# Kernel tuning notes

Hardware: AMD Instinct MI355X
Metric: run time of the kernel (lower is better)

The kernel has to match this reference:

```python
import jax, jax.numpy as jnp
import numpy as np

EPS = 1e-8
TAU = 0.2
IOU_THR = 0.5
NEG = -1e9
N, C, H, D_FG, D_CLS = 8192, 1024, 256, 64, 128


def setup_inputs() -> dict:
    key = jax.random.key(0)
    ks = jax.random.split(key, 11)
    def lin(k, fan_in, fan_out):
        return jax.random.normal(k, (fan_in, fan_out), jnp.float32) / np.sqrt(fan_in)
    return {
        "roi_feats": jax.random.normal(ks[0], (N, C), jnp.float32),
        "labels": jax.random.randint(ks[1], (N,), 0, 21, jnp.int32).astype(jnp.int64),
        "ious": jax.random.uniform(ks[2], (N,), jnp.float32),
        "fg_w1": lin(ks[3], C, H), "fg_b1": jnp.zeros((H,), jnp.float32),
        "fg_w2": lin(ks[4], H, D_FG), "fg_b2": jnp.zeros((D_FG,), jnp.float32),
        "cls_w1": lin(ks[5], C, H), "cls_b1": jnp.zeros((H,), jnp.float32),
        "cls_w2": lin(ks[6], H, D_CLS), "cls_b2": jnp.zeros((D_CLS,), jnp.float32),
    }


def _project_normalize(x, w1, b1, w2, b2):
    h = jax.nn.relu(x @ w1 + b1)
    z = h @ w2 + b2
    norm = jnp.maximum(jnp.linalg.norm(z, axis=1, keepdims=True), EPS)
    return z / norm


def _forward(roi_feats, labels, ious, fg_w1, fg_b1, fg_w2, fg_b2, cls_w1, cls_b1, cls_w2, cls_b2):
    n = roi_feats.shape[0]
    z_fg = _project_normalize(roi_feats, fg_w1, fg_b1, fg_w2, fg_b2)
    z_cls = _project_normalize(roi_feats, cls_w1, cls_b1, cls_w2, cls_b2)

    ignore = labels == -1
    fg = (labels > 0) & ~ignore
    iou_weight = jnp.where(ious > IOU_THR, ious, 0.0)
    eye = jnp.eye(n, dtype=bool)

    # ---- fg/bg contrastive (bg_as_negatives_only=True) ----
    sim_fg = (z_fg @ z_fg.T) / TAU                       # [N,N]
    exp_sim = jnp.exp(sim_fg)
    denom = jnp.sum(exp_sim * (~eye).astype(jnp.float32), axis=1)
    pos = (fg & ~ignore)[None, :] & ~eye                 # positives: fg columns, no self
    n_pos = jnp.sum(pos, axis=1)
    numer = jnp.sum(exp_sim * pos.astype(jnp.float32), axis=1)
    # original computes den = denom + EPS then -log((numer+EPS)/(den+EPS))
    loss_i = -jnp.log((numer + EPS) / (denom + 2.0 * EPS))
    valid = (fg & ~ignore) & (n_pos > 0)
    w = iou_weight * valid.astype(jnp.float32)
    loss_fg_bg = jnp.sum(w * loss_i) / (jnp.sum(w) + EPS)

    # ---- class supervised contrastive ----
    sim_cls = (z_cls @ z_cls.T) / TAU
    sim_masked = jnp.where(eye, NEG, sim_cls)
    log_denom = jax.nn.logsumexp(sim_masked, axis=1)     # [N]
    log_p = jnp.where(eye, NEG, sim_cls - log_denom[:, None])
    # pos_mask keeps diagonal (as in original): same label, col not ignore, col label != 0
    posc = (labels[None, :] == labels[:, None]) & (~ignore)[None, :] & (labels[None, :] != 0)
    n_posc = jnp.sum(posc, axis=1).astype(jnp.float32)
    sum_log_p = jnp.sum(log_p * posc.astype(jnp.float32), axis=1)
    valid_c = (fg & ~ignore) & (n_posc > 0) & jnp.isfinite(log_denom)
    Lzi = jnp.where(valid_c, -sum_log_p / (n_posc + EPS), 0.0)
    wc = iou_weight * valid_c.astype(jnp.float32)
    loss_supcon = jnp.sum(wc * Lzi) / (jnp.sum(wc) + EPS)

    return jnp.stack([loss_fg_bg, loss_supcon])


def reference(roi_feats, labels, ious, fg_w1, fg_b1, fg_w2, fg_b2, cls_w1, cls_b1, cls_w2, cls_b2):
    return _forward(roi_feats, labels, ious, fg_w1, fg_b1, fg_w2, fg_b2, cls_w1, cls_b1, cls_w2, cls_b2)
```

## Files before the change

### kernel.cpp

```cpp
#include <hip/hip_runtime.h>


typedef __attribute__((ext_vector_type(8))) short bs8;
typedef __attribute__((ext_vector_type(4))) float f4;

#define MFMA_BF16(a, b, c) __builtin_amdgcn_mfma_f32_16x16x32_bf16((a), (b), (c), 0, 0, 0)

#if defined(__has_builtin)
#if __has_builtin(__builtin_amdgcn_exp2f)
#define EXP2F(x) __builtin_amdgcn_exp2f(x)
#endif
#endif
#ifndef EXP2F
#define EXP2F(x) exp2f(x)
#endif

#define K_LOG2E 7.2134752044448170f

__device__ __forceinline__ unsigned short f2bf(float f) {
  unsigned int u = __float_as_uint(f);
  u = (u + 0x7fffu + ((u >> 16) & 1u)) >> 16;
  return (unsigned short)u;
}
__device__ __forceinline__ float bf2f(unsigned short s) {
  return __uint_as_float(((unsigned int)s) << 16);
}

constexpr size_t O_W1T  = 0;
constexpr size_t O_W2TF = 1048576;
constexpr size_t O_W2TC = 1081344;
constexpr size_t O_H    = 1146880;
constexpr size_t O_ZF   = 9535488;
constexpr size_t O_ZC   = 10584064;
constexpr size_t O_SCLS = 12681216;
constexpr size_t O_ROWD = 12697600;
constexpr size_t O_ROWN = 12730368;
constexpr size_t O_ROWS = 12763136;
constexpr size_t O_SCAL = 12795904;
constexpr size_t O_HIST = 12795920;
constexpr size_t O_NFG  = 12796048;
constexpr int ZERO_WORDS = (int)((O_SCAL + 16 - O_SCLS) / 4);

__global__ void __launch_bounds__(256) prep_kernel(
    const float* __restrict__ fgw1, const float* __restrict__ clsw1,
    const float* __restrict__ fgw2, const float* __restrict__ clsw2,
    const int* __restrict__ labels,
    unsigned short* __restrict__ W1T, unsigned short* __restrict__ W2Tf,
    unsigned short* __restrict__ W2Tc,
    int* __restrict__ hist, int* __restrict__ nfg, float* __restrict__ zp) {
  const int b = blockIdx.x;
  const int t = threadIdx.x;

  if (b >= 141) {
    const int i = (b - 141) * 256 + t;
    if (i < ZERO_WORDS) zp[i] = 0.f;
    return;
  }
  if (b == 140) {
    __shared__ int sh[33];
    if (t < 33) sh[t] = 0;
    __syncthreads();
    for (int it = 0; it < 32; it++) {
      const int lab = labels[it * 256 + t];
      if (lab >= 0 && lab < 32) atomicAdd(&sh[lab], 1);
      if (lab > 0) atomicAdd(&sh[32], 1);
    }
    __syncthreads();
    if (t < 32) hist[t] = sh[t];
    if (t == 32) *nfg = sh[32];
    return;
  }
  int m, tb;
  if (b < 64)       { m = 0; tb = b; }
  else if (b < 128) { m = 1; tb = b - 64; }
  else if (b < 132) { m = 2; tb = b - 128; }
  else              { m = 3; tb = b - 132; }
  __shared__ float tile[64][65];
  const float* src;
  unsigned short* dst;
  int R, C;
  if (m == 0)      { src = fgw1;  dst = W1T;              R = 1024; C = 256; }
  else if (m == 1) { src = clsw1; dst = W1T + 256 * 1024; R = 1024; C = 256; }
  else if (m == 2) { src = fgw2;  dst = W2Tf;             R = 256;  C = 64;  }
  else             { src = clsw2; dst = W2Tc;             R = 256;  C = 128; }
  const int cT = C >> 6;
  const int r0 = (tb / cT) << 6, c0 = (tb % cT) << 6;
  {
    const int rr = t >> 4, cc = (t & 15) << 2;
#pragma unroll
    for (int i = 0; i < 4; i++) {
      float4 v = *(const float4*)(src + (size_t)(r0 + rr + i * 16) * C + c0 + cc);
      tile[rr + i * 16][cc] = v.x; tile[rr + i * 16][cc + 1] = v.y;
      tile[rr + i * 16][cc + 2] = v.z; tile[rr + i * 16][cc + 3] = v.w;
    }
  }
  __syncthreads();
  {
    const int dr = t >> 2, dc = (t & 3) << 4;
    bs8 o0, o1;
#pragma unroll
    for (int j = 0; j < 8; j++) o0[j] = (short)f2bf(tile[dc + j][dr]);
#pragma unroll
    for (int j = 0; j < 8; j++) o1[j] = (short)f2bf(tile[dc + 8 + j][dr]);
    unsigned short* dp = dst + (size_t)(c0 + dr) * R + r0 + dc;
    *(bs8*)dp = o0;
    *(bs8*)(dp + 8) = o1;
  }
}

__global__ void __launch_bounds__(256) gemm1_kernel(
    const float* __restrict__ X, const unsigned short* __restrict__ W1T,
    const float* __restrict__ b1f, const float* __restrict__ b1c,
    unsigned short* __restrict__ H) {
  __shared__ __align__(16) unsigned short lA[64 * 72];
  __shared__ __align__(16) unsigned short lB[128 * 72];
  const int t = threadIdx.x;
  const int w = t >> 6, lane = t & 63, ln = lane & 15, quad = lane >> 4;
  const int m0 = blockIdx.x * 64, n0 = blockIdx.y * 128;

  const int ar = t >> 2, ac = (t & 3) * 16;
  const int br = t >> 1, bc = (t & 1) * 32;
  const float* xbase = X + (size_t)(m0 + ar) * 1024 + ac;
  const unsigned short* bbase = W1T + (size_t)(n0 + br) * 1024 + bc;

  float4 xa[4];
  bs8 xb[4];
#pragma unroll
  for (int i = 0; i < 4; i++) xa[i] = *(const float4*)(xbase + i * 4);
#pragma unroll
  for (int i = 0; i < 4; i++) xb[i] = *(const bs8*)(bbase + i * 8);

  f4 acc[8];
#pragma unroll
  for (int s = 0; s < 8; s++) acc[s] = (f4){0.f, 0.f, 0.f, 0.f};

  for (int ks = 0; ks < 16; ks++) {
    {
      unsigned short* ap = &lA[ar * 72 + ac];
#pragma unroll
      for (int i = 0; i < 2; i++) {
        bs8 av;
        av[0] = (short)f2bf(xa[2 * i].x);     av[1] = (short)f2bf(xa[2 * i].y);
        av[2] = (short)f2bf(xa[2 * i].z);     av[3] = (short)f2bf(xa[2 * i].w);
        av[4] = (short)f2bf(xa[2 * i + 1].x); av[5] = (short)f2bf(xa[2 * i + 1].y);
        av[6] = (short)f2bf(xa[2 * i + 1].z); av[7] = (short)f2bf(xa[2 * i + 1].w);
        *(bs8*)(ap + i * 8) = av;
      }
      unsigned short* bp = &lB[br * 72 + bc];
#pragma unroll
      for (int i = 0; i < 4; i++) *(bs8*)(bp + i * 8) = xb[i];
    }
    __syncthreads();
    if (ks < 15) {
      const int k1 = (ks + 1) * 64;
#pragma unroll
      for (int i = 0; i < 4; i++) xa[i] = *(const float4*)(xbase + k1 + i * 4);
#pragma unroll
      for (int i = 0; i < 4; i++) xb[i] = *(const bs8*)(bbase + k1 + i * 8);
    }
#pragma unroll
    for (int kk = 0; kk < 2; kk++) {
      bs8 af = *(const bs8*)&lA[(w * 16 + ln) * 72 + kk * 32 + quad * 8];
#pragma unroll
      for (int s = 0; s < 8; s++) {
        bs8 bf = *(const bs8*)&lB[(s * 16 + ln) * 72 + kk * 32 + quad * 8];
        acc[s] = MFMA_BF16(af, bf, acc[s]);
      }
    }
    __syncthreads();
  }
#pragma unroll
  for (int s = 0; s < 8; s++) {
    const int n = n0 + s * 16 + ln;
    const float b = (n < 256) ? b1f[n] : b1c[n - 256];
#pragma unroll
    for (int r = 0; r < 4; r++) {
      float v = fmaxf(acc[s][r] + b, 0.f);
      H[(size_t)(m0 + w * 16 + quad * 4 + r) * 512 + n] = f2bf(v);
    }
  }
}

__global__ void __launch_bounds__(256) gemm2_kernel(
    const unsigned short* __restrict__ H,
    const unsigned short* __restrict__ W2Tf, const unsigned short* __restrict__ W2Tc,
    const float* __restrict__ b2f, const float* __restrict__ b2c,
    unsigned short* __restrict__ Zf, unsigned short* __restrict__ Zc) {
  const int t = threadIdx.x;
  const int w = t >> 6, lane = t & 63, ln = lane & 15, quad = lane >> 4;
  const int rw = blockIdx.x * 32 + (w & 1) * 16;

  if (w < 2) {
    const unsigned short* hrow = H + (size_t)(rw + ln) * 512;
    f4 acc[4];
#pragma unroll
    for (int s = 0; s < 4; s++) acc[s] = (f4){0.f, 0.f, 0.f, 0.f};
#pragma unroll
    for (int ks = 0; ks < 8; ks++) {
      bs8 af = *(const bs8*)(hrow + ks * 32 + quad * 8);
#pragma unroll
      for (int s = 0; s < 4; s++) {
        bs8 bf = *(const bs8*)(W2Tf + (size_t)(s * 16 + ln) * 256 + ks * 32 + quad * 8);
        acc[s] = MFMA_BF16(af, bf, acc[s]);
      }
    }
    float ss[4] = {0.f, 0.f, 0.f, 0.f};
#pragma unroll
    for (int s = 0; s < 4; s++) {
      float b = b2f[s * 16 + ln];
#pragma unroll
      for (int r = 0; r < 4; r++) {
        acc[s][r] += b;
        ss[r] = fmaf(acc[s][r], acc[s][r], ss[r]);
      }
    }
#pragma unroll
    for (int r = 0; r < 4; r++) {
#pragma unroll
      for (int off = 1; off < 16; off <<= 1) ss[r] += __shfl_xor(ss[r], off, 64);
      float sc = 1.f / fmaxf(sqrtf(ss[r]), 1e-8f);
#pragma unroll
      for (int s = 0; s < 4; s++)
        Zf[(size_t)(rw + quad * 4 + r) * 64 + s * 16 + ln] = f2bf(acc[s][r] * sc);
    }
  } else {
    const unsigned short* hrow = H + (size_t)(rw + ln) * 512 + 256;
    f4 acc[8];
#pragma unroll
    for (int s = 0; s < 8; s++) acc[s] = (f4){0.f, 0.f, 0.f, 0.f};
#pragma unroll
    for (int ks = 0; ks < 8; ks++) {
      bs8 af = *(const bs8*)(hrow + ks * 32 + quad * 8);
#pragma unroll
      for (int s = 0; s < 8; s++) {
        bs8 bf = *(const bs8*)(W2Tc + (size_t)(s * 16 + ln) * 256 + ks * 32 + quad * 8);
        acc[s] = MFMA_BF16(af, bf, acc[s]);
      }
    }
    float ss[4] = {0.f, 0.f, 0.f, 0.f};
#pragma unroll
    for (int s = 0; s < 8; s++) {
      float b = b2c[s * 16 + ln];
#pragma unroll
      for (int r = 0; r < 4; r++) {
        acc[s][r] += b;
        ss[r] = fmaf(acc[s][r], acc[s][r], ss[r]);
      }
    }
#pragma unroll
    for (int r = 0; r < 4; r++) {
#pragma unroll
      for (int off = 1; off < 16; off <<= 1) ss[r] += __shfl_xor(ss[r], off, 64);
      float sc = 1.f / fmaxf(sqrtf(ss[r]), 1e-8f);
#pragma unroll
      for (int s = 0; s < 8; s++)
        Zc[(size_t)(rw + quad * 4 + r) * 128 + s * 16 + ln] = f2bf(acc[s][r] * sc);
    }
  }
}

__global__ void __launch_bounds__(128) scls_kernel(const unsigned short* __restrict__ Zc,
                                                   const int* __restrict__ labels,
                                                   float* __restrict__ Scls) {
  const int c = blockIdx.x + 1;
  const int t = threadIdx.x;
  const int r0 = blockIdx.y * 256;
  float acc = 0.f;
#pragma unroll 4
  for (int r = r0; r < r0 + 256; r++) {
    if (labels[r] == c) acc += bf2f(Zc[(size_t)r * 128 + t]);
  }
  atomicAdd(&Scls[c * 128 + t], acc);
}

__global__ void __launch_bounds__(256) simfg_kernel(
    const unsigned short* __restrict__ Zf, const int* __restrict__ labels,
    float* __restrict__ rowD, float* __restrict__ rowN) {
  const int bi = blockIdx.x, d = blockIdx.y;
  if (d == 32 && bi >= 32) return;
  const int bj = (bi + d) & 63;
  const bool diag = (d == 0);

  __shared__ __align__(16) unsigned short sZf[64 * 72];
  __shared__ float sFg[64];
  __shared__ float sCol[4][2][4][16][2];
  const int t = threadIdx.x;
  const int w = t >> 6, lane = t & 63, ln = lane & 15, quad = lane >> 4;
  const int rbase = bi * 128 + w * 32;

  bs8 afg[2][2];
  float fgr[2][4];
#pragma unroll
  for (int rs = 0; rs < 2; rs++) {
    const unsigned short* zf = Zf + (size_t)(rbase + rs * 16 + ln) * 64;
#pragma unroll
    for (int s = 0; s < 2; s++) afg[rs][s] = *(const bs8*)(zf + s * 32 + quad * 8);
#pragma unroll
    for (int r = 0; r < 4; r++)
      fgr[rs][r] = (labels[rbase + rs * 16 + quad * 4 + r] > 0) ? 1.f : 0.f;
  }

  float dacc[2][4] = {}, nacc[2][4] = {};
  float cd[2][4] = {}, cn[2][4] = {};

#pragma unroll
  for (int ct = 0; ct < 2; ct++) {
    const int c0 = bj * 128 + ct * 64;
    __syncthreads();
#pragma unroll
    for (int i = 0; i < 2; i++) {
      int ch = t + i * 256;
      int j = ch >> 3, c8 = (ch & 7) * 8;
      *(bs8*)&sZf[j * 72 + c8] = *(const bs8*)(Zf + (size_t)(c0 + j) * 64 + c8);
    }
    if (t < 64) sFg[t] = (labels[c0 + t] > 0) ? 1.f : 0.f;
    __syncthreads();

#pragma unroll
    for (int s = 0; s < 4; s++) {
      const int lcol = s * 16 + ln;
      const float fgc = sFg[lcol];
      bs8 b0 = *(const bs8*)&sZf[lcol * 72 + quad * 8];
      bs8 b1 = *(const bs8*)&sZf[lcol * 72 + 32 + quad * 8];
#pragma unroll
      for (int rs = 0; rs < 2; rs++) {
        f4 c = {0.f, 0.f, 0.f, 0.f};
        c = MFMA_BF16(afg[rs][0], b0, c);
        c = MFMA_BF16(afg[rs][1], b1, c);
#pragma unroll
        for (int r = 0; r < 4; r++) {
          float e = EXP2F(c[r] * K_LOG2E);
          dacc[rs][r] += e;
          nacc[rs][r] = fmaf(fgc, e, nacc[rs][r]);
          cd[ct][s] += e;
          cn[ct][s] = fmaf(fgr[rs][r], e, cn[ct][s]);
        }
      }
    }
  }

  if (!diag) {
#pragma unroll
    for (int ct = 0; ct < 2; ct++)
#pragma unroll
      for (int s = 0; s < 4; s++) {
        float dv = cd[ct][s], nv = cn[ct][s];
#pragma unroll
        for (int off = 16; off < 64; off <<= 1) {
          dv += __shfl_xor(dv, off, 64);
          nv += __shfl_xor(nv, off, 64);
        }
        if (quad == 0) {
          sCol[w][ct][s][ln][0] = dv;
          sCol[w][ct][s][ln][1] = nv;
        }
      }
    __syncthreads();
    if (t < 128) {
      const int ct = t >> 6, s = (t >> 4) & 3, lm = t & 15;
      float dv = 0.f, nv = 0.f;
#pragma unroll
      for (int ww = 0; ww < 4; ww++) {
        dv += sCol[ww][ct][s][lm][0];
        nv += sCol[ww][ct][s][lm][1];
      }
      const int col = bj * 128 + t;
      atomicAdd(&rowD[col], dv);
      atomicAdd(&rowN[col], nv);
    }
  }

#pragma unroll
  for (int rs = 0; rs < 2; rs++)
#pragma unroll
    for (int r = 0; r < 4; r++) {
      float dv = dacc[rs][r], nv = nacc[rs][r];
#pragma unroll
      for (int off = 1; off < 16; off <<= 1) {
        dv += __shfl_xor(dv, off, 64);
        nv += __shfl_xor(nv, off, 64);
      }
      if (ln == 0) {
        int row = rbase + rs * 16 + quad * 4 + r;
        atomicAdd(&rowD[row], dv);
        atomicAdd(&rowN[row], nv);
      }
    }
}

__global__ void __launch_bounds__(256) simcls_kernel(
    const unsigned short* __restrict__ Zc, float* __restrict__ rowS) {
  const int bi = blockIdx.x, d = blockIdx.y;
  if (d == 32 && bi >= 32) return;
  const int bj = (bi + d) & 63;
  const bool diag = (d == 0);

  __shared__ __align__(16) unsigned short sZc[64 * 136];
  __shared__ float sCol[4][2][4][16];
  const int t = threadIdx.x;
  const int w = t >> 6, lane = t & 63, ln = lane & 15, quad = lane >> 4;
  const int rbase = bi * 128 + w * 32;

  bs8 acl[2][4];
#pragma unroll
  for (int rs = 0; rs < 2; rs++) {
    const unsigned short* zc = Zc + (size_t)(rbase + rs * 16 + ln) * 128;
#pragma unroll
    for (int s = 0; s < 4; s++) acl[rs][s] = *(const bs8*)(zc + s * 32 + quad * 8);
  }

  float sacc[2][4] = {};
  float cs[2][4] = {};

#pragma unroll
  for (int ct = 0; ct < 2; ct++) {
    const int c0 = bj * 128 + ct * 64;
    __syncthreads();
#pragma unroll
    for (int i = 0; i < 4; i++) {
      int ch = t + i * 256;
      int j = ch >> 4, c8 = (ch & 15) * 8;
      *(bs8*)&sZc[j * 136 + c8] = *(const bs8*)(Zc + (size_t)(c0 + j) * 128 + c8);
    }
    __syncthreads();

#pragma unroll
    for (int s = 0; s < 4; s++) {
      const int lcol = s * 16 + ln;
      bs8 bc0 = *(const bs8*)&sZc[lcol * 136 + quad * 8];
      bs8 bc1 = *(const bs8*)&sZc[lcol * 136 + 32 + quad * 8];
      bs8 bc2 = *(const bs8*)&sZc[lcol * 136 + 64 + quad * 8];
      bs8 bc3 = *(const bs8*)&sZc[lcol * 136 + 96 + quad * 8];
#pragma unroll
      for (int rs = 0; rs < 2; rs++) {
        f4 c = {0.f, 0.f, 0.f, 0.f};
        c = MFMA_BF16(acl[rs][0], bc0, c);
        c = MFMA_BF16(acl[rs][1], bc1, c);
        c = MFMA_BF16(acl[rs][2], bc2, c);
        c = MFMA_BF16(acl[rs][3], bc3, c);
#pragma unroll
        for (int r = 0; r < 4; r++) {
          float e = EXP2F(c[r] * K_LOG2E);
          sacc[rs][r] += e;
          cs[ct][s] += e;
        }
      }
    }
  }

  if (!diag) {
#pragma unroll
    for (int ct = 0; ct < 2; ct++)
#pragma unroll
      for (int s = 0; s < 4; s++) {
        float sv = cs[ct][s];
#pragma unroll
        for (int off = 16; off < 64; off <<= 1) sv += __shfl_xor(sv, off, 64);
        if (quad == 0) sCol[w][ct][s][ln] = sv;
      }
    __syncthreads();
    if (t < 128) {
      const int ct = t >> 6, s = (t >> 4) & 3, lm = t & 15;
      float sv = 0.f;
#pragma unroll
      for (int ww = 0; ww < 4; ww++) sv += sCol[ww][ct][s][lm];
      atomicAdd(&rowS[bj * 128 + t], sv);
    }
  }

#pragma unroll
  for (int rs = 0; rs < 2; rs++)
#pragma unroll
    for (int r = 0; r < 4; r++) {
      float sv = sacc[rs][r];
#pragma unroll
      for (int off = 1; off < 16; off <<= 1) sv += __shfl_xor(sv, off, 64);
      if (ln == 0)
        atomicAdd(&rowS[rbase + rs * 16 + quad * 4 + r], sv);
    }
}

__global__ void __launch_bounds__(256) finalize_kernel(
    const unsigned short* __restrict__ Zf, const unsigned short* __restrict__ Zc,
    const int* __restrict__ labels, const float* __restrict__ ious,
    const float* __restrict__ rowD, const float* __restrict__ rowN,
    const float* __restrict__ rowS, const float* __restrict__ Scls,
    const int* __restrict__ hist, const int* __restrict__ nfg,
    float* __restrict__ scal) {
  __shared__ float red[4][4];
  const int t = threadIdx.x, w = t >> 6, lane = t & 63;
  float aw0 = 0.f, al0 = 0.f, aw1 = 0.f, al1 = 0.f;
  const int NFG = *nfg;
  for (int it = 0; it < 16; it++) {
    const int i = it * 512 + blockIdx.x * 4 + w;
    const int lab = labels[i];
    if (lab > 0 && lab < 32) {
      const float iou = ious[i];
      const float iw = (iou > 0.5f) ? iou : 0.f;
      float dot = 0.f, ssq = 0.f;
#pragma unroll
      for (int p = 0; p < 2; p++) {
        const int k = lane + p * 64;
        const float z = bf2f(Zc[(size_t)i * 128 + k]);
        dot = fmaf(z, Scls[lab * 128 + k], dot);
        ssq = fmaf(z, z, ssq);
      }
      float zf = bf2f(Zf[(size_t)i * 64 + lane]);
      float ssqf = zf * zf;
#pragma unroll
      for (int off = 1; off < 64; off <<= 1) {
        dot += __shfl_xor(dot, off, 64);
        ssq += __shfl_xor(ssq, off, 64);
        ssqf += __shfl_xor(ssqf, off, 64);
      }
      if (lane == 0) {
        const float ef = EXP2F(K_LOG2E * ssqf);
        if (NFG - 1 > 0) {
          const float D = rowD[i] - ef;
          const float Nn = rowN[i] - ef;
          const float loss = logf(D + 2e-8f) - logf(Nn + 1e-8f);
          aw0 += iw;
          al0 += iw * loss;
        }
        const int npc = hist[lab];
        if (npc > 0) {
          const float S = rowS[i] - EXP2F(K_LOG2E * ssq);
          const float logden = logf(S);
          const float slp = (dot - ssq) * 5.0f - (float)(npc - 1) * logden - 1e9f;
          aw1 += iw;
          al1 += iw * (-slp / ((float)npc + 1e-8f));
        }
      }
    }
  }
  if (lane == 0) { red[w][0] = aw0; red[w][1] = al0; red[w][2] = aw1; red[w][3] = al1; }
  __syncthreads();
  if (t < 4) atomicAdd(&scal[t], red[0][t] + red[1][t] + red[2][t] + red[3][t]);
}

__global__ void writeout_kernel(const float* __restrict__ scal, float* __restrict__ out) {
  if (threadIdx.x == 0) {
    out[0] = scal[1] / (scal[0] + 1e-8f);
    out[1] = scal[3] / (scal[2] + 1e-8f);
  }
}

extern "C" void kernel_launch(void* const* d_in, const int* in_sizes, int n_in,
                              void* d_out, int out_size, void* d_ws, size_t ws_size,
                              hipStream_t stream) {
  (void)in_sizes; (void)n_in; (void)out_size; (void)ws_size;
  const float* roi    = (const float*)d_in[0];
  const int*   labels = (const int*)d_in[1];
  const float* ious   = (const float*)d_in[2];
  const float* fgw1   = (const float*)d_in[3];
  const float* fgb1   = (const float*)d_in[4];
  const float* fgw2   = (const float*)d_in[5];
  const float* fgb2   = (const float*)d_in[6];
  const float* clsw1  = (const float*)d_in[7];
  const float* clsb1  = (const float*)d_in[8];
  const float* clsw2  = (const float*)d_in[9];
  const float* clsb2  = (const float*)d_in[10];

  char* ws = (char*)d_ws;
  unsigned short* W1T  = (unsigned short*)(ws + O_W1T);
  unsigned short* W2Tf = (unsigned short*)(ws + O_W2TF);
  unsigned short* W2Tc = (unsigned short*)(ws + O_W2TC);
  unsigned short* Hb   = (unsigned short*)(ws + O_H);
  unsigned short* Zf   = (unsigned short*)(ws + O_ZF);
  unsigned short* Zc   = (unsigned short*)(ws + O_ZC);
  float* Scls = (float*)(ws + O_SCLS);
  float* rowD = (float*)(ws + O_ROWD);
  float* rowN = (float*)(ws + O_ROWN);
  float* rowS = (float*)(ws + O_ROWS);
  float* scal = (float*)(ws + O_SCAL);
  int* hist = (int*)(ws + O_HIST);
  int* nfg  = (int*)(ws + O_NFG);
  float* out = (float*)d_out;

  hipLaunchKernelGGL(prep_kernel, dim3(254), dim3(256), 0, stream,
                     fgw1, clsw1, fgw2, clsw2, labels, W1T, W2Tf, W2Tc,
                     hist, nfg, (float*)(ws + O_SCLS));
  hipLaunchKernelGGL(gemm1_kernel, dim3(128, 4), dim3(256), 0, stream,
                     roi, W1T, fgb1, clsb1, Hb);
  hipLaunchKernelGGL(gemm2_kernel, dim3(256), dim3(256), 0, stream,
                     Hb, W2Tf, W2Tc, fgb2, clsb2, Zf, Zc);
  hipLaunchKernelGGL(scls_kernel, dim3(20, 32), dim3(128), 0, stream, Zc, labels, Scls);
  hipLaunchKernelGGL(simfg_kernel, dim3(64, 33), dim3(256), 0, stream,
                     Zf, labels, rowD, rowN);
  hipLaunchKernelGGL(simcls_kernel, dim3(64, 33), dim3(256), 0, stream, Zc, rowS);
  hipLaunchKernelGGL(finalize_kernel, dim3(128), dim3(256), 0, stream,
                     Zf, Zc, labels, ious, rowD, rowN, rowS, Scls, hist, nfg, scal);
  hipLaunchKernelGGL(writeout_kernel, dim3(1), dim3(64), 0, stream, scal, out);
}
```

Baseline: 212.4 us.

## Merge fg and cls similarity kernels into one launch and widen gemm1 blocks

The two N×N similarity kernels (fg and class) become one kernel with a doubled grid. Blocks branch on blockIdx.y and reuse a shared-memory arena sized for the larger path. This removes one launch and lets both workloads run on the GPU together, at the cost of a larger LDS footprint for the fg blocks. Separately, gemm1 now uses 512 threads per block with 8 waves split as 4 row groups by 2 column halves, halving per-thread accumulators and loads to raise the number of waves in flight.

```diff
diff --git a/kernel.cpp b/kernel.cpp
--- a/kernel.cpp
+++ b/kernel.cpp
@@ -108,7 +108,7 @@
   }
 }
 
-__global__ void __launch_bounds__(256) gemm1_kernel(
+__global__ void __launch_bounds__(512) gemm1_kernel(
     const float* __restrict__ X, const unsigned short* __restrict__ W1T,
     const float* __restrict__ b1f, const float* __restrict__ b1c,
     unsigned short* __restrict__ H) {
@@ -116,67 +116,64 @@
   __shared__ __align__(16) unsigned short lB[128 * 72];
   const int t = threadIdx.x;
   const int w = t >> 6, lane = t & 63, ln = lane & 15, quad = lane >> 4;
+  const int wr = (w & 3) * 16, wc = (w >> 2) * 64;
   const int m0 = blockIdx.x * 64, n0 = blockIdx.y * 128;
 
-  const int ar = t >> 2, ac = (t & 3) * 16;
-  const int br = t >> 1, bc = (t & 1) * 32;
+  const int ar = t >> 3, ac = (t & 7) * 8;
+  const int br = t >> 2, bc = (t & 3) * 16;
   const float* xbase = X + (size_t)(m0 + ar) * 1024 + ac;
   const unsigned short* bbase = W1T + (size_t)(n0 + br) * 1024 + bc;
 
-  float4 xa[4];
-  bs8 xb[4];
-#pragma unroll
-  for (int i = 0; i < 4; i++) xa[i] = *(const float4*)(xbase + i * 4);
-#pragma unroll
-  for (int i = 0; i < 4; i++) xb[i] = *(const bs8*)(bbase + i * 8);
-
-  f4 acc[8];
-#pragma unroll
-  for (int s = 0; s < 8; s++) acc[s] = (f4){0.f, 0.f, 0.f, 0.f};
+  float4 xa[2];
+  bs8 xb[2];
+#pragma unroll
+  for (int i = 0; i < 2; i++) xa[i] = *(const float4*)(xbase + i * 4);
+#pragma unroll
+  for (int i = 0; i < 2; i++) xb[i] = *(const bs8*)(bbase + i * 8);
+
+  f4 acc[4];
+#pragma unroll
+  for (int s = 0; s < 4; s++) acc[s] = (f4){0.f, 0.f, 0.f, 0.f};
 
   for (int ks = 0; ks < 16; ks++) {
     {
-      unsigned short* ap = &lA[ar * 72 + ac];
-#pragma unroll
-      for (int i = 0; i < 2; i++) {
-        bs8 av;
-        av[0] = (short)f2bf(xa[2 * i].x);     av[1] = (short)f2bf(xa[2 * i].y);
-        av[2] = (short)f2bf(xa[2 * i].z);     av[3] = (short)f2bf(xa[2 * i].w);
-        av[4] = (short)f2bf(xa[2 * i + 1].x); av[5] = (short)f2bf(xa[2 * i + 1].y);
-        av[6] = (short)f2bf(xa[2 * i + 1].z); av[7] = (short)f2bf(xa[2 * i + 1].w);
-        *(bs8*)(ap + i * 8) = av;
-      }
+      bs8 av;
+      av[0] = (short)f2bf(xa[0].x); av[1] = (short)f2bf(xa[0].y);
+      av[2] = (short)f2bf(xa[0].z); av[3] = (short)f2bf(xa[0].w);
+      av[4] = (short)f2bf(xa[1].x); av[5] = (short)f2bf(xa[1].y);
+      av[6] = (short)f2bf(xa[1].z); av[7] = (short)f2bf(xa[1].w);
+      *(bs8*)&lA[ar * 72 + ac] = av;
       unsigned short* bp = &lB[br * 72 + bc];
-#pragma unroll
-      for (int i = 0; i < 4; i++) *(bs8*)(bp + i * 8) = xb[i];
+      *(bs8*)(bp) = xb[0];
+      *(bs8*)(bp + 8) = xb[1];
     }
     __syncthreads();
     if (ks < 15) {
       const int k1 = (ks + 1) * 64;
 #pragma unroll
-      for (int i = 0; i < 4; i++) xa[i] = *(const float4*)(xbase + k1 + i * 4);
-#pragma unroll
-      for (int i = 0; i < 4; i++) xb[i] = *(const bs8*)(bbase + k1 + i * 8);
+      for (int i = 0; i < 2; i++) xa[i] = *(const float4*)(xbase + k1 + i * 4);
+#pragma unroll
+      for (int i = 0; i < 2; i++) xb[i] = *(const bs8*)(bbase + k1 + i * 8);
     }
 #pragma unroll
     for (int kk = 0; kk < 2; kk++) {
-      bs8 af = *(const bs8*)&lA[(w * 16 + ln) * 72 + kk * 32 + quad * 8];
-#pragma unroll
-      for (int s = 0; s < 8; s++) {
-        bs8 bf = *(const bs8*)&lB[(s * 16 + ln) * 72 + kk * 32 + quad * 8];
+      bs8 af = *(const bs8*)&lA[(wr + ln) * 72 + kk * 32 + quad * 8];
+#pragma unroll
+      for (int s = 0; s < 4; s++) {
+        bs8 bf = *(const bs8*)&lB[(wc + s * 16 + ln) * 72 + kk * 32 + quad * 8];
         acc[s] = MFMA_BF16(af, bf, acc[s]);
       }
     }
     __syncthreads();
   }
 #pragma unroll
-  for (int s = 0; s < 8; s++) {
-    const int n = n0 + s * 16 + ln;
+  for (int s = 0; s < 4; s++) {
+    const int n = n0 + wc + s * 16 + ln;
     const float b = (n < 256) ? b1f[n] : b1c[n - 256];
 #pragma unroll
     for (int r = 0; r < 4; r++) {
       float v = fmaxf(acc[s][r] + b, 0.f);
-      H[(size_t)(m0 + w * 16 + quad * 4 + r) * 512 + n] = f2bf(v);
+      H[(size_t)(m0 + wr + quad * 4 + r) * 512 + n] = f2bf(v);
     }
   }
 }
@@ -273,211 +270,209 @@
   atomicAdd(&Scls[c * 128 + t], acc);
 }
 
-__global__ void __launch_bounds__(256) simfg_kernel(
-    const unsigned short* __restrict__ Zf, const int* __restrict__ labels,
-    float* __restrict__ rowD, float* __restrict__ rowN) {
-  const int bi = blockIdx.x, d = blockIdx.y;
+__global__ void __launch_bounds__(256) sim2_kernel(
+    const unsigned short* __restrict__ Zf, const unsigned short* __restrict__ Zc,
+    const int* __restrict__ labels,
+    float* __restrict__ rowD, float* __restrict__ rowN, float* __restrict__ rowS) {
+  const int bi = blockIdx.x, y = blockIdx.y;
+  const bool isfg = (y <= 32);
+  const int d = isfg ? y : y - 33;
   if (d == 32 && bi >= 32) return;
   const int bj = (bi + d) & 63;
   const bool diag = (d == 0);
 
-  __shared__ __align__(16) unsigned short sZf[64 * 72];
-  __shared__ float sFg[64];
-  __shared__ float sCol[4][2][4][16][2];
+  __shared__ __align__(16) char arena[19712];
   const int t = threadIdx.x;
   const int w = t >> 6, lane = t & 63, ln = lane & 15, quad = lane >> 4;
   const int rbase = bi * 128 + w * 32;
 
-  bs8 afg[2][2];
-  float fgr[2][4];
-#pragma unroll
-  for (int rs = 0; rs < 2; rs++) {
-    const unsigned short* zf = Zf + (size_t)(rbase + rs * 16 + ln) * 64;
-#pragma unroll
-    for (int s = 0; s < 2; s++) afg[rs][s] = *(const bs8*)(zf + s * 32 + quad * 8);
-#pragma unroll
-    for (int r = 0; r < 4; r++)
-      fgr[rs][r] = (labels[rbase + rs * 16 + quad * 4 + r] > 0) ? 1.f : 0.f;
-  }
-
-  float dacc[2][4] = {}, nacc[2][4] = {};
-  float cd[2][4] = {}, cn[2][4] = {};
-
-#pragma unroll
-  for (int ct = 0; ct < 2; ct++) {
-    const int c0 = bj * 128 + ct * 64;
-    __syncthreads();
-#pragma unroll
-    for (int i = 0; i < 2; i++) {
-      int ch = t + i * 256;
-      int j = ch >> 3, c8 = (ch & 7) * 8;
-      *(bs8*)&sZf[j * 72 + c8] = *(const bs8*)(Zf + (size_t)(c0 + j) * 64 + c8);
-    }
-    if (t < 64) sFg[t] = (labels[c0 + t] > 0) ? 1.f : 0.f;
-    __syncthreads();
-
-#pragma unroll
-    for (int s = 0; s < 4; s++) {
-      const int lcol = s * 16 + ln;
-      const float fgc = sFg[lcol];
-      bs8 b0 = *(const bs8*)&sZf[lcol * 72 + quad * 8];
-      bs8 b1 = *(const bs8*)&sZf[lcol * 72 + 32 + quad * 8];
-#pragma unroll
-      for (int rs = 0; rs < 2; rs++) {
-        f4 c = {0.f, 0.f, 0.f, 0.f};
-        c = MFMA_BF16(afg[rs][0], b0, c);
-        c = MFMA_BF16(afg[rs][1], b1, c);
-#pragma unroll
-        for (int r = 0; r < 4; r++) {
-          float e = EXP2F(c[r] * K_LOG2E);
-          dacc[rs][r] += e;
-          nacc[rs][r] = fmaf(fgc, e, nacc[rs][r]);
-          cd[ct][s] += e;
-          cn[ct][s] = fmaf(fgr[rs][r], e, cn[ct][s]);
-        }
-      }
-    }
-  }
-
-  if (!diag) {
-#pragma unroll
-    for (int ct = 0; ct < 2; ct++)
+  if (isfg) {
+    unsigned short* sZf = (unsigned short*)arena;
+    float* sFg = (float*)(arena + 9216);
+    float* sCol = (float*)(arena + 9472);
+
+    bs8 afg[2][2];
+    float fgr[2][4];
+#pragma unroll
+    for (int rs = 0; rs < 2; rs++) {
+      const unsigned short* zf = Zf + (size_t)(rbase + rs * 16 + ln) * 64;
+#pragma unroll
+      for (int s = 0; s < 2; s++) afg[rs][s] = *(const bs8*)(zf + s * 32 + quad * 8);
+#pragma unroll
+      for (int r = 0; r < 4; r++)
+        fgr[rs][r] = (labels[rbase + rs * 16 + quad * 4 + r] > 0) ? 1.f : 0.f;
+    }
+
+    float dacc[2][4] = {}, nacc[2][4] = {};
+    float cd[2][4] = {}, cn[2][4] = {};
+
+#pragma unroll
+    for (int ct = 0; ct < 2; ct++) {
+      const int c0 = bj * 128 + ct * 64;
+      __syncthreads();
+#pragma unroll
+      for (int i = 0; i < 2; i++) {
+        int ch = t + i * 256;
+        int j = ch >> 3, c8 = (ch & 7) * 8;
+        *(bs8*)&sZf[j * 72 + c8] = *(const bs8*)(Zf + (size_t)(c0 + j) * 64 + c8);
+      }
+      if (t < 64) sFg[t] = (labels[c0 + t] > 0) ? 1.f : 0.f;
+      __syncthreads();
+
 #pragma unroll
       for (int s = 0; s < 4; s++) {
-        float dv = cd[ct][s], nv = cn[ct][s];
-#pragma unroll
-        for (int off = 16; off < 64; off <<= 1) {
+        const int lcol = s * 16 + ln;
+        const float fgc = sFg[lcol];
+        bs8 b0 = *(const bs8*)&sZf[lcol * 72 + quad * 8];
+        bs8 b1 = *(const bs8*)&sZf[lcol * 72 + 32 + quad * 8];
+#pragma unroll
+        for (int rs = 0; rs < 2; rs++) {
+          f4 c = {0.f, 0.f, 0.f, 0.f};
+          c = MFMA_BF16(afg[rs][0], b0, c);
+          c = MFMA_BF16(afg[rs][1], b1, c);
+#pragma unroll
+          for (int r = 0; r < 4; r++) {
+            float e = EXP2F(c[r] * K_LOG2E);
+            dacc[rs][r] += e;
+            nacc[rs][r] = fmaf(fgc, e, nacc[rs][r]);
+            cd[ct][s] += e;
+            cn[ct][s] = fmaf(fgr[rs][r], e, cn[ct][s]);
+          }
+        }
+      }
+    }
+
+    if (!diag) {
+#pragma unroll
+      for (int ct = 0; ct < 2; ct++)
+#pragma unroll
+        for (int s = 0; s < 4; s++) {
+          float dv = cd[ct][s], nv = cn[ct][s];
+#pragma unroll
+          for (int off = 16; off < 64; off <<= 1) {
+            dv += __shfl_xor(dv, off, 64);
+            nv += __shfl_xor(nv, off, 64);
+          }
+          if (quad == 0) {
+            const int idx = (((w * 2 + ct) * 4 + s) * 16 + ln) * 2;
+            sCol[idx] = dv;
+            sCol[idx + 1] = nv;
+          }
+        }
+      __syncthreads();
+      if (t < 128) {
+        const int ct = t >> 6, s = (t >> 4) & 3, lm = t & 15;
+        float dv = 0.f, nv = 0.f;
+#pragma unroll
+        for (int ww = 0; ww < 4; ww++) {
+          const int idx = (((ww * 2 + ct) * 4 + s) * 16 + lm) * 2;
+          dv += sCol[idx];
+          nv += sCol[idx + 1];
+        }
+        const int col = bj * 128 + t;
+        atomicAdd(&rowD[col], dv);
+        atomicAdd(&rowN[col], nv);
+      }
+    }
+
+#pragma unroll
+    for (int rs = 0; rs < 2; rs++)
+#pragma unroll
+      for (int r = 0; r < 4; r++) {
+        float dv = dacc[rs][r], nv = nacc[rs][r];
+#pragma unroll
+        for (int off = 1; off < 16; off <<= 1) {
           dv += __shfl_xor(dv, off, 64);
           nv += __shfl_xor(nv, off, 64);
         }
-        if (quad == 0) {
-          sCol[w][ct][s][ln][0] = dv;
-          sCol[w][ct][s][ln][1] = nv;
-        }
-      }
-    __syncthreads();
-    if (t < 128) {
-      const int ct = t >> 6, s = (t >> 4) & 3, lm = t & 15;
-      float dv = 0.f, nv = 0.f;
-#pragma unroll
-      for (int ww = 0; ww < 4; ww++) {
-        dv += sCol[ww][ct][s][lm][0];
-        nv += sCol[ww][ct][s][lm][1];
-      }
-      const int col = bj * 128 + t;
-      atomicAdd(&rowD[col], dv);
-      atomicAdd(&rowN[col], nv);
-    }
-  }
-
-#pragma unroll
-  for (int rs = 0; rs < 2; rs++)
-#pragma unroll
-    for (int r = 0; r < 4; r++) {
-      float dv = dacc[rs][r], nv = nacc[rs][r];
-#pragma unroll
-      for (int off = 1; off < 16; off <<= 1) {
-        dv += __shfl_xor(dv, off, 64);
-        nv += __shfl_xor(nv, off, 64);
-      }
-      if (ln == 0) {
-        int row = rbase + rs * 16 + quad * 4 + r;
-        atomicAdd(&rowD[row], dv);
-        atomicAdd(&rowN[row], nv);
-      }
-    }
-}
-
-__global__ void __launch_bounds__(256) simcls_kernel(
-    const unsigned short* __restrict__ Zc, float* __restrict__ rowS) {
-  const int bi = blockIdx.x, d = blockIdx.y;
-  if (d == 32 && bi >= 32) return;
-  const int bj = (bi + d) & 63;
-  const bool diag = (d == 0);
-
-  __shared__ __align__(16) unsigned short sZc[64 * 136];
-  __shared__ float sCol[4][2][4][16];
-  const int t = threadIdx.x;
-  const int w = t >> 6, lane = t & 63, ln = lane & 15, quad = lane >> 4;
-  const int rbase = bi * 128 + w * 32;
-
-  bs8 acl[2][4];
-#pragma unroll
-  for (int rs = 0; rs < 2; rs++) {
-    const unsigned short* zc = Zc + (size_t)(rbase + rs * 16 + ln) * 128;
-#pragma unroll
-    for (int s = 0; s < 4; s++) acl[rs][s] = *(const bs8*)(zc + s * 32 + quad * 8);
-  }
-
-  float sacc[2][4] = {};
-  float cs[2][4] = {};
-
-#pragma unroll
-  for (int ct = 0; ct < 2; ct++) {
-    const int c0 = bj * 128 + ct * 64;
-    __syncthreads();
-#pragma unroll
-    for (int i = 0; i < 4; i++) {
-      int ch = t + i * 256;
-      int j = ch >> 4, c8 = (ch & 15) * 8;
-      *(bs8*)&sZc[j * 136 + c8] = *(const bs8*)(Zc + (size_t)(c0 + j) * 128 + c8);
-    }
-    __syncthreads();
-
-#pragma unroll
-    for (int s = 0; s < 4; s++) {
-      const int lcol = s * 16 + ln;
-      bs8 bc0 = *(const bs8*)&sZc[lcol * 136 + quad * 8];
-      bs8 bc1 = *(const bs8*)&sZc[lcol * 136 + 32 + quad * 8];
-      bs8 bc2 = *(const bs8*)&sZc[lcol * 136 + 64 + quad * 8];
-      bs8 bc3 = *(const bs8*)&sZc[lcol * 136 + 96 + quad * 8];
-#pragma unroll
-      for (int rs = 0; rs < 2; rs++) {
-        f4 c = {0.f, 0.f, 0.f, 0.f};
-        c = MFMA_BF16(acl[rs][0], bc0, c);
-        c = MFMA_BF16(acl[rs][1], bc1, c);
-        c = MFMA_BF16(acl[rs][2], bc2, c);
-        c = MFMA_BF16(acl[rs][3], bc3, c);
-#pragma unroll
-        for (int r = 0; r < 4; r++) {
-          float e = EXP2F(c[r] * K_LOG2E);
-          sacc[rs][r] += e;
-          cs[ct][s] += e;
-        }
-      }
-    }
-  }
-
-  if (!diag) {
-#pragma unroll
-    for (int ct = 0; ct < 2; ct++)
+        if (ln == 0) {
+          int row = rbase + rs * 16 + quad * 4 + r;
+          atomicAdd(&rowD[row], dv);
+          atomicAdd(&rowN[row], nv);
+        }
+      }
+  } else {
+    unsigned short* sZc = (unsigned short*)arena;
+    float* sCol = (float*)(arena + 17408);
+
+    bs8 acl[2][4];
+#pragma unroll
+    for (int rs = 0; rs < 2; rs++) {
+      const unsigned short* zc = Zc + (size_t)(rbase + rs * 16 + ln) * 128;
+#pragma unroll
+      for (int s = 0; s < 4; s++) acl[rs][s] = *(const bs8*)(zc + s * 32 + quad * 8);
+    }
+
+    float sacc[2][4] = {};
+    float cs[2][4] = {};
+
+#pragma unroll
+    for (int ct = 0; ct < 2; ct++) {
+      const int c0 = bj * 128 + ct * 64;
+      __syncthreads();
+#pragma unroll
+      for (int i = 0; i < 4; i++) {
+        int ch = t + i * 256;
+        int j = ch >> 4, c8 = (ch & 15) * 8;
+        *(bs8*)&sZc[j * 136 + c8] = *(const bs8*)(Zc + (size_t)(c0 + j) * 128 + c8);
+      }
+      __syncthreads();
+
 #pragma unroll
       for (int s = 0; s < 4; s++) {
-        float sv = cs[ct][s];
-#pragma unroll
-        for (int off = 16; off < 64; off <<= 1) sv += __shfl_xor(sv, off, 64);
-        if (quad == 0) sCol[w][ct][s][ln] = sv;
-      }
-    __syncthreads();
-    if (t < 128) {
-      const int ct = t >> 6, s = (t >> 4) & 3, lm = t & 15;
-      float sv = 0.f;
-#pragma unroll
-      for (int ww = 0; ww < 4; ww++) sv += sCol[ww][ct][s][lm];
-      atomicAdd(&rowS[bj * 128 + t], sv);
-    }
-  }
-
-#pragma unroll
-  for (int rs = 0; rs < 2; rs++)
-#pragma unroll
-    for (int r = 0; r < 4; r++) {
-      float sv = sacc[rs][r];
-#pragma unroll
-      for (int off = 1; off < 16; off <<= 1) sv += __shfl_xor(sv, off, 64);
-      if (ln == 0)
-        atomicAdd(&rowS[rbase + rs * 16 + quad * 4 + r], sv);
-    }
+        const int lcol = s * 16 + ln;
+        bs8 bc0 = *(const bs8*)&sZc[lcol * 136 + quad * 8];
+        bs8 bc1 = *(const bs8*)&sZc[lcol * 136 + 32 + quad * 8];
+        bs8 bc2 = *(const bs8*)&sZc[lcol * 136 + 64 + quad * 8];
+        bs8 bc3 = *(const bs8*)&sZc[lcol * 136 + 96 + quad * 8];
+#pragma unroll
+        for (int rs = 0; rs < 2; rs++) {
+          f4 c = {0.f, 0.f, 0.f, 0.f};
+          c = MFMA_BF16(acl[rs][0], bc0, c);
+          c = MFMA_BF16(acl[rs][1], bc1, c);
+          c = MFMA_BF16(acl[rs][2], bc2, c);
+          c = MFMA_BF16(acl[rs][3], bc3, c);
+#pragma unroll
+          for (int r = 0; r < 4; r++) {
+            float e = EXP2F(c[r] * K_LOG2E);
+            sacc[rs][r] += e;
+            cs[ct][s] += e;
+          }
+        }
+      }
+    }
+
+    if (!diag) {
+#pragma unroll
+      for (int ct = 0; ct < 2; ct++)
+#pragma unroll
+        for (int s = 0; s < 4; s++) {
+          float sv = cs[ct][s];
+#pragma unroll
+          for (int off = 16; off < 64; off <<= 1) sv += __shfl_xor(sv, off, 64);
+          if (quad == 0) sCol[((w * 2 + ct) * 4 + s) * 16 + ln] = sv;
+        }
+      __syncthreads();
+      if (t < 128) {
+        const int ct = t >> 6, s = (t >> 4) & 3, lm = t & 15;
+        float sv = 0.f;
+#pragma unroll
+        for (int ww = 0; ww < 4; ww++) sv += sCol[((ww * 2 + ct) * 4 + s) * 16 + lm];
+        atomicAdd(&rowS[bj * 128 + t], sv);
+      }
+    }
+
+#pragma unroll
+    for (int rs = 0; rs < 2; rs++)
+#pragma unroll
+      for (int r = 0; r < 4; r++) {
+        float sv = sacc[rs][r];
+#pragma unroll
+        for (int off = 1; off < 16; off <<= 1) sv += __shfl_xor(sv, off, 64);
+        if (ln == 0)
+          atomicAdd(&rowS[rbase + rs * 16 + quad * 4 + r], sv);
+      }
+  }
 }
 
 __global__ void __launch_bounds__(256) finalize_kernel(
@@ -580,14 +575,13 @@
   hipLaunchKernelGGL(prep_kernel, dim3(254), dim3(256), 0, stream,
                      fgw1, clsw1, fgw2, clsw2, labels, W1T, W2Tf, W2Tc,
                      hist, nfg, (float*)(ws + O_SCLS));
-  hipLaunchKernelGGL(gemm1_kernel, dim3(128, 4), dim3(256), 0, stream,
+  hipLaunchKernelGGL(gemm1_kernel, dim3(128, 4), dim3(512), 0, stream,
                      roi, W1T, fgb1, clsb1, Hb);
   hipLaunchKernelGGL(gemm2_kernel, dim3(256), dim3(256), 0, stream,
                      Hb, W2Tf, W2Tc, fgb2, clsb2, Zf, Zc);
   hipLaunchKernelGGL(scls_kernel, dim3(20, 32), dim3(128), 0, stream, Zc, labels, Scls);
-  hipLaunchKernelGGL(simfg_kernel, dim3(64, 33), dim3(256), 0, stream,
-                     Zf, labels, rowD, rowN);
-  hipLaunchKernelGGL(simcls_kernel, dim3(64, 33), dim3(256), 0, stream, Zc, rowS);
+  hipLaunchKernelGGL(sim2_kernel, dim3(64, 66), dim3(256), 0, stream,
+                     Zf, Zc, labels, rowD, rowN, rowS);
   hipLaunchKernelGGL(finalize_kernel, dim3(128), dim3(256), 0, stream,
                      Zf, Zc, labels, ious, rowD, rowN, rowS, Scls, hist, nfg, scal);
   hipLaunchKernelGGL(writeout_kernel, dim3(1), dim3(64), 0, stream, scal, out);
```

Result: no change. 208.4 us (-1.9%).
